# Performance work log

Hardware: AMD Instinct MI355X
Metric: run time of the kernel (lower is better)

Reference implementation:

```python
import jax, jax.numpy as jnp
import numpy as np

ALPHA = 0.3  # keras LeakyReLU default

def leaky(x):
    return jnp.where(x >= 0, x, ALPHA * x)

def setup_inputs() -> dict:
    key = jax.random.key(0)
    ks = jax.random.split(key, 16)
    T, B, E, H = 200, 64, 64, 64
    scale = 0.05  # 'random_normal' init
    d = {}
    d["inputs"] = jax.random.normal(ks[0], (T, B, E), jnp.float32)
    d["w1_k"] = jax.random.normal(ks[1], (E, H), jnp.float32) * scale
    d["w1_b"] = jnp.zeros((H,), jnp.float32)
    d["w2_k"] = jax.random.normal(ks[2], (E, H), jnp.float32) * scale
    d["w3_k"] = jax.random.normal(ks[3], (E, H), jnp.float32) * scale
    d["w0_k"] = jax.random.normal(ks[4], (H,), jnp.float32) * scale
    # prediction MLPs: two towers (a on m_a, b on inputs) x 2 layers, for 'c' and 'v'
    dims = [(E, 64), (64, 32)]
    i = 5
    for pref in ["pc", "pv"]:
        for li, (din, dout) in enumerate(dims):
            for side in ["a", "b"]:
                d[f"{pref}_{side}{li}_k"] = jax.random.normal(ks[i], (din, dout), jnp.float32) * scale
                d[f"{pref}_{side}{li}_b"] = jnp.zeros((dout,), jnp.float32)
                i += 1
    return d

def _mlp(x, layers):
    # Dense + LeakyReLU per layer (dropout inactive at inference: training=False)
    for k, b in layers:
        x = leaky(x @ k + b)
    return x

def reference(inputs, w1_k, w1_b, w2_k, w3_k, w0_k,
              pc_a0_k, pc_a0_b, pc_b0_k, pc_b0_b, pc_a1_k, pc_a1_b, pc_b1_k, pc_b1_b,
              pv_a0_k, pv_a0_b, pv_b0_k, pv_b0_b, pv_a1_k, pv_a1_b, pv_b1_k, pv_b1_b):
    T = inputs.shape[0]
    # running mean over time: m_s[i] = mean(inputs[:i+1])
    m_s = jnp.cumsum(inputs, axis=0) / (jnp.arange(T, dtype=inputs.dtype) + 1.0)[:, None, None]
    x1 = inputs @ w1_k + w1_b          # [T,B,H] keyed by j
    q = inputs @ w2_k + m_s @ w3_k     # [T,B,H] keyed by i (x2[i] + wms[i])
    # scores[i,j,b] = w0 . sigmoid(x1[j] + q[i]); triangular mask j <= i
    s = jnp.einsum('ijbh,h->ijb', jax.nn.sigmoid(x1[None, :] + q[:, None]), w0_k)
    mask = jnp.tril(jnp.ones((T, T), inputs.dtype))
    m_a = jnp.einsum('ijb,jbe->ibe', s * mask[:, :, None], inputs)  # [T,B,E]
    pc = jax.nn.sigmoid(jnp.sum(
        _mlp(m_a, [(pc_a0_k, pc_a0_b), (pc_a1_k, pc_a1_b)]) *
        _mlp(inputs, [(pc_b0_k, pc_b0_b), (pc_b1_k, pc_b1_b)]),
        axis=-1, keepdims=True))
    pv = jax.nn.sigmoid(jnp.sum(
        _mlp(m_a, [(pv_a0_k, pv_a0_b), (pv_a1_k, pv_a1_b)]) *
        _mlp(inputs, [(pv_b0_k, pv_b0_b), (pv_b1_k, pv_b1_b)]),
        axis=-1, keepdims=True))
    pv = pv * pc
    return (pc, pv)
```

## Files before the change

kernel.cpp:

```cpp
#include <hip/hip_runtime.h>
#include <hip/hip_bf16.h>

#define TT 200
#define BB 64
#define TB (TT*BB)
#define NL2E (-1.44269504088896f)

#define C4(v,kk) (((const float*)&(v))[kk])

__device__ __forceinline__ float sigm_fast(float x) {
    return __builtin_amdgcn_rcpf(1.0f + __builtin_amdgcn_exp2f(NL2E * x));
}
__device__ __forceinline__ float leaky(float x) {
    return x >= 0.0f ? x : 0.3f * x;
}

__global__ __launch_bounds__(256) void gemm3_kernel(
    const float* __restrict__ inputs,
    const float* __restrict__ w1k, const float* __restrict__ w1b,
    const float* __restrict__ w2k, const float* __restrict__ w3k,
    float* __restrict__ x1e, float* __restrict__ qbuf, float* __restrict__ y3)
{
    __shared__ __align__(16) float w1s[4096], w2s[4096], w3s[4096], b1s[64];
    __shared__ float4 rows4[4][4][16];
    int t = threadIdx.x;
    for (int i = t; i < 4096; i += 256) { w1s[i] = w1k[i]; w2s[i] = w2k[i]; w3s[i] = w3k[i]; }
    if (t < 64) b1s[t] = w1b[t];
    __syncthreads();
    int wv = t >> 6, lane = t & 63;
    int rr = lane >> 4, k4s = lane & 15;
    for (int r0 = blockIdx.x * 16; r0 < TB; r0 += gridDim.x * 16) {
        int rb = r0 + wv * 4;
        rows4[wv][rr][k4s] = *(const float4*)&inputs[(rb + rr) * 64 + k4s * 4];
        float a1_0 = b1s[lane], a1_1 = b1s[lane], a1_2 = b1s[lane], a1_3 = b1s[lane];
        float a2_0 = 0.f, a2_1 = 0.f, a2_2 = 0.f, a2_3 = 0.f;
        float a3_0 = 0.f, a3_1 = 0.f, a3_2 = 0.f, a3_3 = 0.f;
        #pragma unroll 4
        for (int k4 = 0; k4 < 16; k4++) {
            float4 x0 = rows4[wv][0][k4];
            float4 x1 = rows4[wv][1][k4];
            float4 x2 = rows4[wv][2][k4];
            float4 x3 = rows4[wv][3][k4];
            #pragma unroll
            for (int kk = 0; kk < 4; kk++) {
                int k = k4 * 4 + kk;
                float W1 = w1s[k * 64 + lane];
                float W2 = w2s[k * 64 + lane];
                float W3 = w3s[k * 64 + lane];
                float v0 = C4(x0, kk), v1 = C4(x1, kk), v2 = C4(x2, kk), v3 = C4(x3, kk);
                a1_0 += v0 * W1; a1_1 += v1 * W1; a1_2 += v2 * W1; a1_3 += v3 * W1;
                a2_0 += v0 * W2; a2_1 += v1 * W2; a2_2 += v2 * W2; a2_3 += v3 * W2;
                a3_0 += v0 * W3; a3_1 += v1 * W3; a3_2 += v2 * W3; a3_3 += v3 * W3;
            }
        }
        x1e[(rb    ) * 64 + lane] = __builtin_amdgcn_exp2f(NL2E * a1_0);
        x1e[(rb + 1) * 64 + lane] = __builtin_amdgcn_exp2f(NL2E * a1_1);
        x1e[(rb + 2) * 64 + lane] = __builtin_amdgcn_exp2f(NL2E * a1_2);
        x1e[(rb + 3) * 64 + lane] = __builtin_amdgcn_exp2f(NL2E * a1_3);
        qbuf[(rb    ) * 64 + lane] = a2_0;
        qbuf[(rb + 1) * 64 + lane] = a2_1;
        qbuf[(rb + 2) * 64 + lane] = a2_2;
        qbuf[(rb + 3) * 64 + lane] = a2_3;
        y3[(rb    ) * 64 + lane] = a3_0;
        y3[(rb + 1) * 64 + lane] = a3_1;
        y3[(rb + 2) * 64 + lane] = a3_2;
        y3[(rb + 3) * 64 + lane] = a3_3;
    }
}

__global__ __launch_bounds__(256) void cumsum_kernel(
    const float* __restrict__ y3, float* __restrict__ qe)
{
    __shared__ float part[4][64];
    int b = blockIdx.x, t = threadIdx.x;
    int c = t >> 6, h = t & 63;
    int base = b * 64 + h;
    const int L = 50;
    int t0 = c * L;
    float vals[L];
    float s = 0.f;
    #pragma unroll
    for (int i = 0; i < L; i++) {
        vals[i] = y3[(t0 + i) * 4096 + base];
        s += vals[i];
    }
    part[c][h] = s;
    __syncthreads();
    float acc = 0.f;
    #pragma unroll
    for (int cc = 0; cc < 3; cc++) acc += (cc < c) ? part[cc][h] : 0.f;
    #pragma unroll
    for (int i = 0; i < L; i++) {
        int tt = t0 + i;
        int idx = tt * 4096 + base;
        acc += vals[i];
        float q = qe[idx] + acc / (float)(tt + 1);
        qe[idx] = __builtin_amdgcn_exp2f(NL2E * q);
    }
}

__global__ __launch_bounds__(256) void scores_kernel(
    const float* __restrict__ x1e, const float* __restrict__ qe,
    const float* __restrict__ inputs, const float* __restrict__ w0k,
    float* __restrict__ m_a)
{
    __shared__ __align__(16) float xt[32 * 68];
    __shared__ __align__(16) float pt[32 * 68];
    __shared__ __align__(16) float St2[32 * 36];
    __shared__ __align__(16) float w0s[64];
    int t = threadIdx.x;
    int b = blockIdx.x, it = 6 - blockIdx.y;
    int i0 = it * 32;
    int ilA = t & 31, jg = t >> 5;

    float4 qreg[16];
    {
        int gq = i0 + ilA; if (gq > TT - 1) gq = TT - 1;
        const float* qrow = qe + gq * 4096 + b * 64;
        #pragma unroll
        for (int h4 = 0; h4 < 16; h4++) qreg[h4] = *(const float4*)&qrow[h4 * 4];
    }
    if (t < 64) w0s[t] = w0k[t];

    int wv = t >> 6, e = t & 63;
    int il0 = wv * 8;
    float acc[8] = {0.f,0.f,0.f,0.f,0.f,0.f,0.f,0.f};

    for (int jt = 0; jt <= it; jt++) {
        int j0 = jt * 32;
        __syncthreads();
        for (int i = t; i < 2048; i += 256) {
            int r = i >> 6, h = i & 63;
            int gj = j0 + r;
            bool v = (gj < TT);
            xt[r * 68 + h] = v ? x1e[gj * 4096 + b * 64 + h] : 0.f;
            pt[r * 68 + h] = v ? inputs[gj * 4096 + b * 64 + h] : 0.f;
        }
        __syncthreads();
        float s0 = 0.f, s1 = 0.f, s2 = 0.f, s3 = 0.f;
        #pragma unroll 4
        for (int h4 = 0; h4 < 16; h4++) {
            float4 q4 = qreg[h4];
            float4 w4 = *(const float4*)&w0s[h4 * 4];
            float4 xA = *(const float4*)&xt[(jg     ) * 68 + h4 * 4];
            float4 xB = *(const float4*)&xt[(jg +  8) * 68 + h4 * 4];
            float4 xC = *(const float4*)&xt[(jg + 16) * 68 + h4 * 4];
            float4 xD = *(const float4*)&xt[(jg + 24) * 68 + h4 * 4];
            #pragma unroll
            for (int kk = 0; kk < 4; kk++) {
                float qv = C4(q4, kk), w = C4(w4, kk);
                s0 += w * __builtin_amdgcn_rcpf(1.f + qv * C4(xA, kk));
                s1 += w * __builtin_amdgcn_rcpf(1.f + qv * C4(xB, kk));
                s2 += w * __builtin_amdgcn_rcpf(1.f + qv * C4(xC, kk));
                s3 += w * __builtin_amdgcn_rcpf(1.f + qv * C4(xD, kk));
            }
        }
        {
            int gi = i0 + ilA, gj = j0 + jg;
            St2[(jg     ) * 36 + ilA] = (gj      <= gi && gi < TT) ? s0 : 0.f;
            St2[(jg +  8) * 36 + ilA] = (gj +  8 <= gi && gi < TT) ? s1 : 0.f;
            St2[(jg + 16) * 36 + ilA] = (gj + 16 <= gi && gi < TT) ? s2 : 0.f;
            St2[(jg + 24) * 36 + ilA] = (gj + 24 <= gi && gi < TT) ? s3 : 0.f;
        }
        __syncthreads();
        #pragma unroll 4
        for (int jl = 0; jl < 32; jl++) {
            float v = pt[jl * 68 + e];
            float4 sA = *(const float4*)&St2[jl * 36 + il0];
            float4 sB = *(const float4*)&St2[jl * 36 + il0 + 4];
            acc[0] += C4(sA,0) * v; acc[1] += C4(sA,1) * v;
            acc[2] += C4(sA,2) * v; acc[3] += C4(sA,3) * v;
            acc[4] += C4(sB,0) * v; acc[5] += C4(sB,1) * v;
            acc[6] += C4(sB,2) * v; acc[7] += C4(sB,3) * v;
        }
    }
    #pragma unroll
    for (int k2 = 0; k2 < 8; k2++) {
        int gi = i0 + il0 + k2;
        if (gi < TT) m_a[gi * 4096 + b * 64 + e] = acc[k2];
    }
}

__global__ __launch_bounds__(256) void mlp2_kernel(
    const float* __restrict__ ma, const float* __restrict__ inputs,
    const float* __restrict__ pc_a0k, const float* __restrict__ pc_a0b,
    const float* __restrict__ pc_b0k, const float* __restrict__ pc_b0b,
    const float* __restrict__ pc_a1k, const float* __restrict__ pc_a1b,
    const float* __restrict__ pc_b1k, const float* __restrict__ pc_b1b,
    const float* __restrict__ pv_a0k, const float* __restrict__ pv_a0b,
    const float* __restrict__ pv_b0k, const float* __restrict__ pv_b0b,
    const float* __restrict__ pv_a1k, const float* __restrict__ pv_a1b,
    const float* __restrict__ pv_b1k, const float* __restrict__ pv_b1b,
    float* __restrict__ outp)
{
    __shared__ __align__(16) float wA0[4096], wB0[4096];
    __shared__ __align__(16) float acts[4][8][2][64];
    int t = threadIdx.x, wv = t >> 6, lane = t & 63;
    int tw = lane >> 5, h2 = lane & 31;

    auto stage_acts = [&]() {
        float4* a4 = (float4*)&acts[wv][0][0][0];
        #pragma unroll
        for (int p = 0; p < 4; p++) {
            int fw = p * 64 + lane;
            int r = fw >> 5, src = (fw >> 4) & 1, k4 = fw & 15;
            int row = blockIdx.x * 32 + wv * 8 + r;
            const float* sp = src ? inputs : ma;
            a4[fw] = *(const float4*)&sp[row * 64 + k4 * 4];
        }
    };

    stage_acts();
    for (int i = t; i < 4096; i += 256) { wA0[i] = pc_a0k[i]; wB0[i] = pc_b0k[i]; }
    __syncthreads();

    float pcr[8];
    {
        float bA = pc_a0b[lane], bB = pc_b0b[lane];
        float accA[8], accB[8];
        #pragma unroll
        for (int r = 0; r < 8; r++) { accA[r] = bA; accB[r] = bB; }
        #pragma unroll 4
        for (int k4 = 0; k4 < 16; k4++) {
            float4 aA[8], aB[8];
            #pragma unroll
            for (int r = 0; r < 8; r++) {
                aA[r] = *(const float4*)&acts[wv][r][0][k4 * 4];
                aB[r] = *(const float4*)&acts[wv][r][1][k4 * 4];
            }
            #pragma unroll
            for (int kk = 0; kk < 4; kk++) {
                float wAv = wA0[(k4 * 4 + kk) * 64 + lane];
                float wBv = wB0[(k4 * 4 + kk) * 64 + lane];
                #pragma unroll
                for (int r = 0; r < 8; r++) {
                    accA[r] += C4(aA[r], kk) * wAv;
                    accB[r] += C4(aB[r], kk) * wBv;
                }
            }
        }
        #pragma unroll
        for (int r = 0; r < 8; r++) {
            acts[wv][r][0][lane] = leaky(accA[r]);
            acts[wv][r][1][lane] = leaky(accB[r]);
        }
        const float* w1p = tw ? pc_b1k : pc_a1k;
        float b1 = (tw ? pc_b1b : pc_a1b)[h2];
        float o[8];
        #pragma unroll
        for (int r = 0; r < 8; r++) o[r] = b1;
        for (int k = 0; k < 64; k++) {
            float w1 = w1p[k * 32 + h2];
            #pragma unroll
            for (int r = 0; r < 8; r++) o[r] += acts[wv][r][tw][k] * w1;
        }
        #pragma unroll
        for (int r = 0; r < 8; r++) {
            float po = leaky(o[r]);
            float pr = po * __shfl_xor(po, 32);
            #pragma unroll
            for (int m = 1; m <= 16; m <<= 1) pr += __shfl_xor(pr, m);
            pcr[r] = pr;
        }
    }
    __syncthreads();
    for (int i = t; i < 4096; i += 256) { wA0[i] = pv_a0k[i]; wB0[i] = pv_b0k[i]; }
    stage_acts();
    __syncthreads();
    {
        float bA = pv_a0b[lane], bB = pv_b0b[lane];
        float accA[8], accB[8];
        #pragma unroll
        for (int r = 0; r < 8; r++) { accA[r] = bA; accB[r] = bB; }
        #pragma unroll 4
        for (int k4 = 0; k4 < 16; k4++) {
            float4 aA[8], aB[8];
            #pragma unroll
            for (int r = 0; r < 8; r++) {
                aA[r] = *(const float4*)&acts[wv][r][0][k4 * 4];
                aB[r] = *(const float4*)&acts[wv][r][1][k4 * 4];
            }
            #pragma unroll
            for (int kk = 0; kk < 4; kk++) {
                float wAv = wA0[(k4 * 4 + kk) * 64 + lane];
                float wBv = wB0[(k4 * 4 + kk) * 64 + lane];
                #pragma unroll
                for (int r = 0; r < 8; r++) {
                    accA[r] += C4(aA[r], kk) * wAv;
                    accB[r] += C4(aB[r], kk) * wBv;
                }
            }
        }
        #pragma unroll
        for (int r = 0; r < 8; r++) {
            acts[wv][r][0][lane] = leaky(accA[r]);
            acts[wv][r][1][lane] = leaky(accB[r]);
        }
        const float* w1p = tw ? pv_b1k : pv_a1k;
        float b1 = (tw ? pv_b1b : pv_a1b)[h2];
        float o[8];
        #pragma unroll
        for (int r = 0; r < 8; r++) o[r] = b1;
        for (int k = 0; k < 64; k++) {
            float w1 = w1p[k * 32 + h2];
            #pragma unroll
            for (int r = 0; r < 8; r++) o[r] += acts[wv][r][tw][k] * w1;
        }
        #pragma unroll
        for (int r = 0; r < 8; r++) {
            float po = leaky(o[r]);
            float pr = po * __shfl_xor(po, 32);
            #pragma unroll
            for (int m = 1; m <= 16; m <<= 1) pr += __shfl_xor(pr, m);
            if (lane == 0) {
                int row = blockIdx.x * 32 + wv * 8 + r;
                float spc = sigm_fast(pcr[r]);
                outp[row] = spc;
                outp[TB + row] = sigm_fast(pr) * spc;
            }
        }
    }
}

extern "C" void kernel_launch(void* const* d_in, const int* in_sizes, int n_in,
                              void* d_out, int out_size, void* d_ws, size_t ws_size,
                              hipStream_t stream) {
    const float* inputs = (const float*)d_in[0];
    const float* w1k = (const float*)d_in[1];
    const float* w1b = (const float*)d_in[2];
    const float* w2k = (const float*)d_in[3];
    const float* w3k = (const float*)d_in[4];
    const float* w0k = (const float*)d_in[5];
    float* out = (float*)d_out;
    float* ws  = (float*)d_ws;
    float* x1e  = ws;
    float* qbuf = ws + 819200;
    float* y3   = ws + 2 * 819200;
    float* ma   = y3;

    gemm3_kernel<<<dim3(400), 256, 0, stream>>>(inputs, w1k, w1b, w2k, w3k, x1e, qbuf, y3);
    cumsum_kernel<<<dim3(64), 256, 0, stream>>>(y3, qbuf);
    scores_kernel<<<dim3(64, 7), 256, 0, stream>>>(x1e, qbuf, inputs, w0k, ma);
    mlp2_kernel<<<dim3(400), 256, 0, stream>>>(ma, inputs,
        (const float*)d_in[6],  (const float*)d_in[7],  (const float*)d_in[8],  (const float*)d_in[9],
        (const float*)d_in[10], (const float*)d_in[11], (const float*)d_in[12], (const float*)d_in[13],
        (const float*)d_in[14], (const float*)d_in[15], (const float*)d_in[16], (const float*)d_in[17],
        (const float*)d_in[18], (const float*)d_in[19], (const float*)d_in[20], (const float*)d_in[21],
        out);
}
```

Before: 216.6 us.

## Split scores kernel over key tiles with partial m_a slices; widen gemm and cumsum grids

The attention-like scores kernel now splits each query tile's triangular range of key tiles across S blocks. Each block writes a partial m_a slice to workspace, and the MLP kernel sums the slices when it stages activations. This raises block count and evens out the triangular load imbalance, at the cost of extra workspace traffic and a reduction pass. The q tile moves from registers to LDS, and the gemm and cumsum kernels are regridded so each block does one tile or half the channels, adding parallelism.

```diff
diff --git a/kernel.cpp b/kernel.cpp
--- a/kernel.cpp
+++ b/kernel.cpp
@@ -4,6 +4,7 @@
 #define TT 200
 #define BB 64
 #define TB (TT*BB)
+#define SLICE 819200
 #define NL2E (-1.44269504088896f)
 
 #define C4(v,kk) (((const float*)&(v))[kk])
@@ -26,74 +27,67 @@
     int t = threadIdx.x;
     for (int i = t; i < 4096; i += 256) { w1s[i] = w1k[i]; w2s[i] = w2k[i]; w3s[i] = w3k[i]; }
     if (t < 64) b1s[t] = w1b[t];
-    __syncthreads();
     int wv = t >> 6, lane = t & 63;
     int rr = lane >> 4, k4s = lane & 15;
-    for (int r0 = blockIdx.x * 16; r0 < TB; r0 += gridDim.x * 16) {
-        int rb = r0 + wv * 4;
-        rows4[wv][rr][k4s] = *(const float4*)&inputs[(rb + rr) * 64 + k4s * 4];
-        float a1_0 = b1s[lane], a1_1 = b1s[lane], a1_2 = b1s[lane], a1_3 = b1s[lane];
-        float a2_0 = 0.f, a2_1 = 0.f, a2_2 = 0.f, a2_3 = 0.f;
-        float a3_0 = 0.f, a3_1 = 0.f, a3_2 = 0.f, a3_3 = 0.f;
-        #pragma unroll 4
-        for (int k4 = 0; k4 < 16; k4++) {
-            float4 x0 = rows4[wv][0][k4];
-            float4 x1 = rows4[wv][1][k4];
-            float4 x2 = rows4[wv][2][k4];
-            float4 x3 = rows4[wv][3][k4];
-            #pragma unroll
-            for (int kk = 0; kk < 4; kk++) {
-                int k = k4 * 4 + kk;
-                float W1 = w1s[k * 64 + lane];
-                float W2 = w2s[k * 64 + lane];
-                float W3 = w3s[k * 64 + lane];
-                float v0 = C4(x0, kk), v1 = C4(x1, kk), v2 = C4(x2, kk), v3 = C4(x3, kk);
-                a1_0 += v0 * W1; a1_1 += v1 * W1; a1_2 += v2 * W1; a1_3 += v3 * W1;
-                a2_0 += v0 * W2; a2_1 += v1 * W2; a2_2 += v2 * W2; a2_3 += v3 * W2;
-                a3_0 += v0 * W3; a3_1 += v1 * W3; a3_2 += v2 * W3; a3_3 += v3 * W3;
-            }
-        }
-        x1e[(rb    ) * 64 + lane] = __builtin_amdgcn_exp2f(NL2E * a1_0);
-        x1e[(rb + 1) * 64 + lane] = __builtin_amdgcn_exp2f(NL2E * a1_1);
-        x1e[(rb + 2) * 64 + lane] = __builtin_amdgcn_exp2f(NL2E * a1_2);
-        x1e[(rb + 3) * 64 + lane] = __builtin_amdgcn_exp2f(NL2E * a1_3);
-        qbuf[(rb    ) * 64 + lane] = a2_0;
-        qbuf[(rb + 1) * 64 + lane] = a2_1;
-        qbuf[(rb + 2) * 64 + lane] = a2_2;
-        qbuf[(rb + 3) * 64 + lane] = a2_3;
-        y3[(rb    ) * 64 + lane] = a3_0;
-        y3[(rb + 1) * 64 + lane] = a3_1;
-        y3[(rb + 2) * 64 + lane] = a3_2;
-        y3[(rb + 3) * 64 + lane] = a3_3;
-    }
+    int rb = blockIdx.x * 16 + wv * 4;
+    rows4[wv][rr][k4s] = *(const float4*)&inputs[(rb + rr) * 64 + k4s * 4];
+    __syncthreads();
+    float a1_0 = b1s[lane], a1_1 = b1s[lane], a1_2 = b1s[lane], a1_3 = b1s[lane];
+    float a2_0 = 0.f, a2_1 = 0.f, a2_2 = 0.f, a2_3 = 0.f;
+    float a3_0 = 0.f, a3_1 = 0.f, a3_2 = 0.f, a3_3 = 0.f;
+    #pragma unroll 4
+    for (int k4 = 0; k4 < 16; k4++) {
+        float4 x0 = rows4[wv][0][k4];
+        float4 x1 = rows4[wv][1][k4];
+        float4 x2 = rows4[wv][2][k4];
+        float4 x3 = rows4[wv][3][k4];
+        #pragma unroll
+        for (int kk = 0; kk < 4; kk++) {
+            int k = k4 * 4 + kk;
+            float W1 = w1s[k * 64 + lane];
+            float W2 = w2s[k * 64 + lane];
+            float W3 = w3s[k * 64 + lane];
+            float v0 = C4(x0, kk), v1 = C4(x1, kk), v2 = C4(x2, kk), v3 = C4(x3, kk);
+            a1_0 += v0 * W1; a1_1 += v1 * W1; a1_2 += v2 * W1; a1_3 += v3 * W1;
+            a2_0 += v0 * W2; a2_1 += v1 * W2; a2_2 += v2 * W2; a2_3 += v3 * W2;
+            a3_0 += v0 * W3; a3_1 += v1 * W3; a3_2 += v2 * W3; a3_3 += v3 * W3;
+        }
+    }
+    x1e[(rb    ) * 64 + lane] = __builtin_amdgcn_exp2f(NL2E * a1_0);
+    x1e[(rb + 1) * 64 + lane] = __builtin_amdgcn_exp2f(NL2E * a1_1);
+    x1e[(rb + 2) * 64 + lane] = __builtin_amdgcn_exp2f(NL2E * a1_2);
+    x1e[(rb + 3) * 64 + lane] = __builtin_amdgcn_exp2f(NL2E * a1_3);
+    qbuf[(rb    ) * 64 + lane] = a2_0;
+    qbuf[(rb + 1) * 64 + lane] = a2_1;
+    qbuf[(rb + 2) * 64 + lane] = a2_2;
+    qbuf[(rb + 3) * 64 + lane] = a2_3;
+    y3[(rb    ) * 64 + lane] = a3_0;
+    y3[(rb + 1) * 64 + lane] = a3_1;
+    y3[(rb + 2) * 64 + lane] = a3_2;
+    y3[(rb + 3) * 64 + lane] = a3_3;
 }
 
 __global__ __launch_bounds__(256) void cumsum_kernel(
     const float* __restrict__ y3, float* __restrict__ qe)
 {
-    __shared__ float part[4][64];
-    int b = blockIdx.x, t = threadIdx.x;
-    int c = t >> 6, h = t & 63;
+    __shared__ float part[8][32];
+    int t = threadIdx.x;
+    int c = t >> 5, hh = t & 31;
+    int b = blockIdx.x >> 1;
+    int h = ((blockIdx.x & 1) << 5) + hh;
     int base = b * 64 + h;
-    const int L = 50;
+    const int L = 25;
     int t0 = c * L;
-    float vals[L];
     float s = 0.f;
-    #pragma unroll
-    for (int i = 0; i < L; i++) {
-        vals[i] = y3[(t0 + i) * 4096 + base];
-        s += vals[i];
-    }
-    part[c][h] = s;
+    for (int i = 0; i < L; i++) s += y3[(t0 + i) * 4096 + base];
+    part[c][hh] = s;
     __syncthreads();
     float acc = 0.f;
-    #pragma unroll
-    for (int cc = 0; cc < 3; cc++) acc += (cc < c) ? part[cc][h] : 0.f;
-    #pragma unroll
+    for (int cc = 0; cc < c; cc++) acc += part[cc][hh];
     for (int i = 0; i < L; i++) {
         int tt = t0 + i;
         int idx = tt * 4096 + base;
-        acc += vals[i];
+        acc += y3[idx];
         float q = qe[idx] + acc / (float)(tt + 1);
         qe[idx] = __builtin_amdgcn_exp2f(NL2E * q);
     }
@@ -102,82 +96,90 @@
 __global__ __launch_bounds__(256) void scores_kernel(
     const float* __restrict__ x1e, const float* __restrict__ qe,
     const float* __restrict__ inputs, const float* __restrict__ w0k,
-    float* __restrict__ m_a)
+    float* __restrict__ ma, int S)
 {
+    __shared__ __align__(16) float qt[32 * 66];
     __shared__ __align__(16) float xt[32 * 68];
     __shared__ __align__(16) float pt[32 * 68];
     __shared__ __align__(16) float St2[32 * 36];
     __shared__ __align__(16) float w0s[64];
     int t = threadIdx.x;
-    int b = blockIdx.x, it = 6 - blockIdx.y;
+    int b = blockIdx.x;
+    int yy = blockIdx.y;
+    int it = 6 - yy / S;
+    int p  = yy % S;
     int i0 = it * 32;
     int ilA = t & 31, jg = t >> 5;
-
-    float4 qreg[16];
-    {
-        int gq = i0 + ilA; if (gq > TT - 1) gq = TT - 1;
-        const float* qrow = qe + gq * 4096 + b * 64;
-        #pragma unroll
-        for (int h4 = 0; h4 < 16; h4++) qreg[h4] = *(const float4*)&qrow[h4 * 4];
-    }
-    if (t < 64) w0s[t] = w0k[t];
-
     int wv = t >> 6, e = t & 63;
     int il0 = wv * 8;
     float acc[8] = {0.f,0.f,0.f,0.f,0.f,0.f,0.f,0.f};
-
-    for (int jt = 0; jt <= it; jt++) {
-        int j0 = jt * 32;
-        __syncthreads();
-        for (int i = t; i < 2048; i += 256) {
-            int r = i >> 6, h = i & 63;
-            int gj = j0 + r;
-            bool v = (gj < TT);
-            xt[r * 68 + h] = v ? x1e[gj * 4096 + b * 64 + h] : 0.f;
-            pt[r * 68 + h] = v ? inputs[gj * 4096 + b * 64 + h] : 0.f;
-        }
-        __syncthreads();
-        float s0 = 0.f, s1 = 0.f, s2 = 0.f, s3 = 0.f;
-        #pragma unroll 4
-        for (int h4 = 0; h4 < 16; h4++) {
-            float4 q4 = qreg[h4];
-            float4 w4 = *(const float4*)&w0s[h4 * 4];
-            float4 xA = *(const float4*)&xt[(jg     ) * 68 + h4 * 4];
-            float4 xB = *(const float4*)&xt[(jg +  8) * 68 + h4 * 4];
-            float4 xC = *(const float4*)&xt[(jg + 16) * 68 + h4 * 4];
-            float4 xD = *(const float4*)&xt[(jg + 24) * 68 + h4 * 4];
-            #pragma unroll
-            for (int kk = 0; kk < 4; kk++) {
-                float qv = C4(q4, kk), w = C4(w4, kk);
-                s0 += w * __builtin_amdgcn_rcpf(1.f + qv * C4(xA, kk));
-                s1 += w * __builtin_amdgcn_rcpf(1.f + qv * C4(xB, kk));
-                s2 += w * __builtin_amdgcn_rcpf(1.f + qv * C4(xC, kk));
-                s3 += w * __builtin_amdgcn_rcpf(1.f + qv * C4(xD, kk));
-            }
-        }
-        {
-            int gi = i0 + ilA, gj = j0 + jg;
-            St2[(jg     ) * 36 + ilA] = (gj      <= gi && gi < TT) ? s0 : 0.f;
-            St2[(jg +  8) * 36 + ilA] = (gj +  8 <= gi && gi < TT) ? s1 : 0.f;
-            St2[(jg + 16) * 36 + ilA] = (gj + 16 <= gi && gi < TT) ? s2 : 0.f;
-            St2[(jg + 24) * 36 + ilA] = (gj + 24 <= gi && gi < TT) ? s3 : 0.f;
-        }
-        __syncthreads();
-        #pragma unroll 4
-        for (int jl = 0; jl < 32; jl++) {
-            float v = pt[jl * 68 + e];
-            float4 sA = *(const float4*)&St2[jl * 36 + il0];
-            float4 sB = *(const float4*)&St2[jl * 36 + il0 + 4];
-            acc[0] += C4(sA,0) * v; acc[1] += C4(sA,1) * v;
-            acc[2] += C4(sA,2) * v; acc[3] += C4(sA,3) * v;
-            acc[4] += C4(sB,0) * v; acc[5] += C4(sB,1) * v;
-            acc[6] += C4(sB,2) * v; acc[7] += C4(sB,3) * v;
+    float* maP = ma + (size_t)p * SLICE;
+
+    if (p <= it) {
+        for (int i2 = t; i2 < 1024; i2 += 256) {
+            int r = i2 >> 5, c2 = i2 & 31;
+            int gq = i0 + r; if (gq > TT - 1) gq = TT - 1;
+            *(float2*)&qt[r * 66 + c2 * 2] = *(const float2*)&qe[gq * 4096 + b * 64 + c2 * 2];
+        }
+        if (t < 64) w0s[t] = w0k[t];
+
+        for (int jt = p; jt <= it; jt += S) {
+            int j0 = jt * 32;
+            __syncthreads();
+            for (int i4 = t; i4 < 512; i4 += 256) {
+                int r = i4 >> 4, c4 = i4 & 15;
+                int gj = j0 + r;
+                if (gj < TT) {
+                    *(float4*)&xt[r * 68 + c4 * 4] = *(const float4*)&x1e[gj * 4096 + b * 64 + c4 * 4];
+                    *(float4*)&pt[r * 68 + c4 * 4] = *(const float4*)&inputs[gj * 4096 + b * 64 + c4 * 4];
+                } else {
+                    *(float4*)&xt[r * 68 + c4 * 4] = make_float4(0.f, 0.f, 0.f, 0.f);
+                    *(float4*)&pt[r * 68 + c4 * 4] = make_float4(0.f, 0.f, 0.f, 0.f);
+                }
+            }
+            __syncthreads();
+            float s0 = 0.f, s1 = 0.f, s2 = 0.f, s3 = 0.f;
+            #pragma unroll 4
+            for (int h4 = 0; h4 < 16; h4++) {
+                float4 w4 = *(const float4*)&w0s[h4 * 4];
+                float4 xA = *(const float4*)&xt[(jg     ) * 68 + h4 * 4];
+                float4 xB = *(const float4*)&xt[(jg +  8) * 68 + h4 * 4];
+                float4 xC = *(const float4*)&xt[(jg + 16) * 68 + h4 * 4];
+                float4 xD = *(const float4*)&xt[(jg + 24) * 68 + h4 * 4];
+                #pragma unroll
+                for (int kk = 0; kk < 4; kk++) {
+                    float qv = qt[ilA * 66 + h4 * 4 + kk];
+                    float w  = C4(w4, kk);
+                    s0 += w * __builtin_amdgcn_rcpf(1.f + qv * C4(xA, kk));
+                    s1 += w * __builtin_amdgcn_rcpf(1.f + qv * C4(xB, kk));
+                    s2 += w * __builtin_amdgcn_rcpf(1.f + qv * C4(xC, kk));
+                    s3 += w * __builtin_amdgcn_rcpf(1.f + qv * C4(xD, kk));
+                }
+            }
+            {
+                int gi = i0 + ilA, gj = j0 + jg;
+                St2[(jg     ) * 36 + ilA] = (gj      <= gi && gi < TT) ? s0 : 0.f;
+                St2[(jg +  8) * 36 + ilA] = (gj +  8 <= gi && gi < TT) ? s1 : 0.f;
+                St2[(jg + 16) * 36 + ilA] = (gj + 16 <= gi && gi < TT) ? s2 : 0.f;
+                St2[(jg + 24) * 36 + ilA] = (gj + 24 <= gi && gi < TT) ? s3 : 0.f;
+            }
+            __syncthreads();
+            #pragma unroll 4
+            for (int jl = 0; jl < 32; jl++) {
+                float v = pt[jl * 68 + e];
+                float4 sA = *(const float4*)&St2[jl * 36 + il0];
+                float4 sB = *(const float4*)&St2[jl * 36 + il0 + 4];
+                acc[0] += C4(sA,0) * v; acc[1] += C4(sA,1) * v;
+                acc[2] += C4(sA,2) * v; acc[3] += C4(sA,3) * v;
+                acc[4] += C4(sB,0) * v; acc[5] += C4(sB,1) * v;
+                acc[6] += C4(sB,2) * v; acc[7] += C4(sB,3) * v;
+            }
         }
     }
     #pragma unroll
     for (int k2 = 0; k2 < 8; k2++) {
         int gi = i0 + il0 + k2;
-        if (gi < TT) m_a[gi * 4096 + b * 64 + e] = acc[k2];
+        if (gi < TT) maP[gi * 4096 + b * 64 + e] = acc[k2];
     }
 }
 
@@ -191,7 +193,7 @@
     const float* __restrict__ pv_b0k, const float* __restrict__ pv_b0b,
     const float* __restrict__ pv_a1k, const float* __restrict__ pv_a1b,
     const float* __restrict__ pv_b1k, const float* __restrict__ pv_b1b,
-    float* __restrict__ outp)
+    float* __restrict__ outp, int S)
 {
     __shared__ __align__(16) float wA0[4096], wB0[4096];
     __shared__ __align__(16) float acts[4][8][2][64];
@@ -201,12 +203,21 @@
     auto stage_acts = [&]() {
         float4* a4 = (float4*)&acts[wv][0][0][0];
         #pragma unroll
-        for (int p = 0; p < 4; p++) {
-            int fw = p * 64 + lane;
+        for (int p4 = 0; p4 < 4; p4++) {
+            int fw = p4 * 64 + lane;
             int r = fw >> 5, src = (fw >> 4) & 1, k4 = fw & 15;
             int row = blockIdx.x * 32 + wv * 8 + r;
-            const float* sp = src ? inputs : ma;
-            a4[fw] = *(const float4*)&sp[row * 64 + k4 * 4];
+            float4 v;
+            if (src) {
+                v = *(const float4*)&inputs[row * 64 + k4 * 4];
+            } else {
+                v = *(const float4*)&ma[row * 64 + k4 * 4];
+                for (int sl = 1; sl < S; sl++) {
+                    float4 u = *(const float4*)&ma[(size_t)sl * SLICE + row * 64 + k4 * 4];
+                    v.x += u.x; v.y += u.y; v.z += u.z; v.w += u.w;
+                }
+            }
+            a4[fw] = v;
         }
     };
 
@@ -333,18 +344,24 @@
     const float* w0k = (const float*)d_in[5];
     float* out = (float*)d_out;
     float* ws  = (float*)d_ws;
+
+    size_t avail_f = ws_size / 4;
+    int S = 1;
+    if      (avail_f >= (size_t)(2 + 4) * SLICE) S = 4;
+    else if (avail_f >= (size_t)(2 + 2) * SLICE) S = 2;
+
     float* x1e  = ws;
-    float* qbuf = ws + 819200;
-    float* y3   = ws + 2 * 819200;
+    float* qbuf = ws + SLICE;
+    float* y3   = ws + 2 * SLICE;
     float* ma   = y3;
 
-    gemm3_kernel<<<dim3(400), 256, 0, stream>>>(inputs, w1k, w1b, w2k, w3k, x1e, qbuf, y3);
-    cumsum_kernel<<<dim3(64), 256, 0, stream>>>(y3, qbuf);
-    scores_kernel<<<dim3(64, 7), 256, 0, stream>>>(x1e, qbuf, inputs, w0k, ma);
+    gemm3_kernel<<<dim3(800), 256, 0, stream>>>(inputs, w1k, w1b, w2k, w3k, x1e, qbuf, y3);
+    cumsum_kernel<<<dim3(128), 256, 0, stream>>>(y3, qbuf);
+    scores_kernel<<<dim3(64, 7 * S), 256, 0, stream>>>(x1e, qbuf, inputs, w0k, ma, S);
     mlp2_kernel<<<dim3(400), 256, 0, stream>>>(ma, inputs,
         (const float*)d_in[6],  (const float*)d_in[7],  (const float*)d_in[8],  (const float*)d_in[9],
         (const float*)d_in[10], (const float*)d_in[11], (const float*)d_in[12], (const float*)d_in[13],
         (const float*)d_in[14], (const float*)d_in[15], (const float*)d_in[16], (const float*)d_in[17],
         (const float*)d_in[18], (const float*)d_in[19], (const float*)d_in[20], (const float*)d_in[21],
-        out);
-}
+        out, S);
+}
```

After: 176.8 us. 1.23x faster.
